# Optimization experiments

Measured on AMD Instinct MI355X. Metric: run time of the kernel, lower is better.

## Reference

```python
import jax, jax.numpy as jnp
import numpy as np

B, NWORD, HID = 4, 24, 512


def setup_inputs() -> dict:
    key = jax.random.key(0)
    ks = jax.random.split(key, 7)
    H = HID
    scale_in = 1.0 / np.sqrt(H)
    return {
        "seqt": jax.random.normal(ks[0], (B, NWORD, 2 * H), dtype=jnp.float32),
        # ins_input_linearity: Linear(H -> 5H) with bias
        "Wi": jax.random.normal(ks[1], (5 * H, H), dtype=jnp.float32) * scale_in,
        "bi": jnp.zeros((5 * H,), dtype=jnp.float32),
        # ins_state_linearity: Linear(H -> 5H) with bias (bias init: forget slots = 1)
        "Ws": jax.random.normal(ks[2], (5 * H, H), dtype=jnp.float32) * scale_in,
        "bs": jnp.zeros((5 * H,), dtype=jnp.float32).at[H:2 * H].set(1.0),
        # ins_bilinearity: BilinearSimilarity(2H, 2H) -> scalar x^T W y
        "Wbil": jax.random.normal(ks[3], (2 * H, 2 * H), dtype=jnp.float32) * (1.0 / (2.0 * H)),
    }


def reference(seqt, Wi, bi, Ws, bs, Wbil):
    """Inside pass (do_inside) of DioLstm in training mode (soft_sum over splits).

    Chart cell (left, L) covers words [left, left+L]. Returns root v = concat(h, c).
    """
    Bn, n, twoH = seqt.shape
    H = twoH // 2
    # ins_bias buffer: ones on the two forget-gate slots [H:3H]
    ins_bias = jnp.zeros((5 * H,), dtype=seqt.dtype).at[H:3 * H].set(1.0)

    def single(seq):  # seq: [n, 2H]
        chartH = jnp.zeros((n, n, H), seq.dtype).at[:, 0].set(seq[:, :H])
        chartC = jnp.zeros((n, n, H), seq.dtype).at[:, 0].set(seq[:, H:])
        chartS = jnp.zeros((n, n), seq.dtype)  # leaf scores are 0
        for L in range(1, n):  # span length - 1 (static unroll over diagonals)
            P = n - L  # number of spans on this diagonal
            lefts = jnp.arange(P)[:, None]          # [P,1]
            ksplit = jnp.arange(L)[None, :]          # [1,L]
            # left child: (left, k); right child: (left+k+1, L-1-k)
            lH = chartH[lefts, ksplit]; lC = chartC[lefts, ksplit]; lS = chartS[lefts, ksplit]
            ridx = lefts + ksplit + 1
            rlen = jnp.broadcast_to(L - 1 - ksplit, ridx.shape)
            rH = chartH[ridx, rlen]; rC = chartC[ridx, rlen]; rS = chartS[ridx, rlen]
            lv = jnp.concatenate([lH, lC], axis=-1)  # [P,L,2H]
            rv = jnp.concatenate([rH, rC], axis=-1)
            # bilinear compatibility + child scores
            compat = jnp.einsum('pki,ij,pkj->pk', lv, Wbil, rv) + lS + rS  # [P,L]
            # projected_input + projected_state (sum once; gate slices of the sum)
            proj = (lH @ Wi.T + bi + ins_bias) + (rH @ Ws.T + bs)  # [P,L,5H]
            ig, lf, rf, g, og = jnp.split(proj, 5, axis=-1)
            ig = jax.nn.sigmoid(ig); lf = jax.nn.sigmoid(lf); rf = jax.nn.sigmoid(rf)
            g = jnp.tanh(g); og = jax.nn.sigmoid(og)
            mem = lf * lC + rf * rC + ig * g
            h = og * jnp.tanh(mem)  # [P,L,H]
            # soft_sum: torch.tensor(s_set) detaches scores -> stop_gradient on weights
            sw = jax.lax.stop_gradient(compat)
            w = jax.nn.softmax(sw, axis=-1)  # [P,L]
            Hnew = jnp.einsum('pk,pkh->ph', w, h)
            Cnew = jnp.einsum('pk,pkh->ph', w, mem)
            Snew = jnp.sum(w * sw, axis=-1)
            pidx = jnp.arange(P)
            chartH = chartH.at[pidx, L].set(Hnew)
            chartC = chartC.at[pidx, L].set(Cnew)
            chartS = chartS.at[pidx, L].set(Snew)
        # root cell v = concat(h, c)
        return jnp.concatenate([chartH[0, n - 1], chartC[0, n - 1]], axis=0)

    return jax.vmap(single)(seqt)  # [B, 2H]
```

## Files before the change

kernel.cpp:

```cpp
#include <hip/hip_runtime.h>
#include <math.h>

#define NB 4
#define NW 24
#define H 512
#define H2 1024
#define H5 2560
#define NCELL 300
#define NEED_BYTES ((size_t)72<<20)

static float* g_buf = nullptr;
__attribute__((constructor)) static void dio_alloc_ws(){
  (void)hipMalloc((void**)&g_buf, NEED_BYTES);
}

typedef __attribute__((ext_vector_type(8))) short bf16x8;
typedef __attribute__((ext_vector_type(4))) float f32x4;
typedef unsigned short ushort_t;

__device__ __forceinline__ int coff(int l){ return l*NW - (l*(l-1))/2; }
__device__ __forceinline__ float sigm(float x){ return 1.f/(1.f+__expf(-x)); }
__device__ __forceinline__ float ftanh(float x){ return 1.f - 2.f/(__expf(2.f*x)+1.f); }

__device__ __forceinline__ ushort_t f2b(float x){
  unsigned int u = __float_as_uint(x);
  u += 0x7FFF + ((u>>16)&1);
  return (ushort_t)(u>>16);
}
__device__ __forceinline__ float b2f(ushort_t h){
  return __uint_as_float(((unsigned int)h)<<16);
}
__device__ __forceinline__ void split_store(ushort_t* __restrict__ ph,
                                            ushort_t* __restrict__ pl,
                                            size_t idx, float x){
  ushort_t h = f2b(x);
  ph[idx] = h;
  pl[idx] = f2b(x - b2f(h));
}

__device__ __forceinline__ float compat_dot(const float* __restrict__ cU,
                                            const float* __restrict__ cH,
                                            const float* __restrict__ cC,
                                            const float* __restrict__ cS,
                                            int lc, int rc, int lane){
  const float4* U4  = (const float4*)(cU + (size_t)lc*H2);
  const float4* Hr4 = (const float4*)(cH + (size_t)rc*H);
  const float4* Cr4 = (const float4*)(cC + (size_t)rc*H);
  float p = 0.f;
  #pragma unroll
  for (int it=0; it<2; it++){
    float4 u = U4[lane + 64*it], h = Hr4[lane + 64*it];
    p += u.x*h.x + u.y*h.y + u.z*h.z + u.w*h.w;
  }
  #pragma unroll
  for (int it=0; it<2; it++){
    float4 u = U4[128 + lane + 64*it], c = Cr4[lane + 64*it];
    p += u.x*c.x + u.y*c.y + u.z*c.z + u.w*c.w;
  }
  #pragma unroll
  for (int off=32; off>0; off>>=1) p += __shfl_down(p, off);
  return p + cS[lc] + cS[rc];
}

__global__ void k_init(const float* __restrict__ seqt,
                       const float* __restrict__ Wi, const float* __restrict__ Ws,
                       const float* __restrict__ Wbil,
                       ushort_t* __restrict__ WiBh, ushort_t* __restrict__ WiBl,
                       ushort_t* __restrict__ WsBh, ushort_t* __restrict__ WsBl,
                       ushort_t* __restrict__ WbilTh, ushort_t* __restrict__ WbilTl,
                       float* __restrict__ cH, float* __restrict__ cC, float* __restrict__ cS,
                       ushort_t* __restrict__ cHbh, ushort_t* __restrict__ cHbl,
                       ushort_t* __restrict__ cCbh, ushort_t* __restrict__ cCbl){
  const int blk = blockIdx.x, t = threadIdx.x;
  if (blk < 10240){
    int i = blk*256 + t;
    const int n = H5*H;
    if (i < n) split_store(WiBh, WiBl, i, Wi[i]);
    else       split_store(WsBh, WsBl, i-n, Ws[i-n]);
  } else if (blk < 11264){
    __shared__ float tile[32][33];
    int tb = blk - 10240;
    int tr = (tb>>5)*32, tc = (tb&31)*32;
    int tx = t & 31, ty = t >> 5;
    #pragma unroll
    for (int i=0;i<32;i+=8)
      tile[ty+i][tx] = Wbil[(size_t)(tr+ty+i)*H2 + tc+tx];
    __syncthreads();
    #pragma unroll
    for (int i=0;i<32;i+=8)
      split_store(WbilTh, WbilTl, (size_t)(tc+ty+i)*H2 + tr+tx, tile[tx][ty+i]);
  } else {
    int tid = (blk-11264)*256 + t;
    if (tid < NB*NW*H){
      int b = tid/(NW*H); int r = tid%(NW*H); int i = r/H; int d = r%H;
      size_t idx = (size_t)(b*NCELL + i)*H + d;
      float hv = seqt[(size_t)(b*NW+i)*H2 + d];
      float cv = seqt[(size_t)(b*NW+i)*H2 + H + d];
      cH[idx]=hv; cC[idx]=cv;
      split_store(cHbh,cHbl,idx,hv);
      split_store(cCbh,cCbl,idx,cv);
      if (d==0) cS[b*NCELL+i] = 0.f;
    }
  }
}

__device__ __forceinline__ void mfma3(f32x4& acc, bf16x8 ah, bf16x8 al,
                                      bf16x8 bh, bf16x8 bl){
  acc = __builtin_amdgcn_mfma_f32_16x16x32_bf16(ah, bh, acc, 0,0,0);
  acc = __builtin_amdgcn_mfma_f32_16x16x32_bf16(ah, bl, acc, 0,0,0);
  acc = __builtin_amdgcn_mfma_f32_16x16x32_bf16(al, bh, acc, 0,0,0);
}

__global__ void __launch_bounds__(512)
k_projN(const ushort_t* __restrict__ WiBh, const ushort_t* __restrict__ WiBl,
        const ushort_t* __restrict__ WsBh, const ushort_t* __restrict__ WsBl,
        const ushort_t* __restrict__ WbilTh, const ushort_t* __restrict__ WbilTl,
        const float* __restrict__ bi, const float* __restrict__ bs,
        const ushort_t* __restrict__ cHbh, const ushort_t* __restrict__ cHbl,
        const ushort_t* __restrict__ cCbh, const ushort_t* __restrict__ cCbl,
        float* __restrict__ cPI, float* __restrict__ cPS, float* __restrict__ cU,
        int d, int P)
{
  __shared__ f32x4 red[8][64];
  const int t = threadIdx.x, wave = t>>6, lane = t&63;
  const int jt = blockIdx.x;
  const int m0 = blockIdx.y*16;
  const int Mtot = NB*P;
  const int nm = min(16, Mtot-m0);

  int kind, j0;
  if (jt < 160){ kind=0; j0 = jt*16; }
  else if (jt < 320){ kind=1; j0 = (jt-160)*16; }
  else { kind=2; j0 = (jt-320)*16; }

  const int r = lane & 15;
  const int q = lane >> 4;

  int mg = m0 + (r < nm ? r : 0);
  const size_t arow = (size_t)((mg/P)*NCELL + coff(d) + mg%P)*H;

  f32x4 acc = {0.f,0.f,0.f,0.f};

  if (kind < 2){
    const ushort_t* bh_ = (kind==0 ? WiBh : WsBh) + (size_t)(j0+r)*H;
    const ushort_t* bl_ = (kind==0 ? WiBl : WsBl) + (size_t)(j0+r)*H;
    const int ks = wave*64 + q*8;
    bf16x8 fah[2], fal[2], fbh[2], fbl[2];
    #pragma unroll
    for (int s=0;s<2;s++){
      const int ko = ks + s*32;
      fah[s] = *(const bf16x8*)(cHbh + arow + ko);
      fal[s] = *(const bf16x8*)(cHbl + arow + ko);
      fbh[s] = *(const bf16x8*)(bh_ + ko);
      fbl[s] = *(const bf16x8*)(bl_ + ko);
    }
    #pragma unroll
    for (int s=0;s<2;s++) mfma3(acc, fah[s], fal[s], fbh[s], fbl[s]);
  } else {
    const ushort_t* bh_ = WbilTh + (size_t)(j0+r)*H2;
    const ushort_t* bl_ = WbilTl + (size_t)(j0+r)*H2;
    const ushort_t* ah_ = (wave<4 ? cHbh : cCbh) + arow;
    const ushort_t* al_ = (wave<4 ? cHbl : cCbl) + arow;
    const int kg0 = wave*128;
    const int ka0 = kg0 & 511;
    bf16x8 fah[4], fal[4], fbh[4], fbl[4];
    #pragma unroll
    for (int s=0;s<4;s++){
      const int so = s*32 + q*8;
      fah[s] = *(const bf16x8*)(ah_ + ka0 + so);
      fal[s] = *(const bf16x8*)(al_ + ka0 + so);
      fbh[s] = *(const bf16x8*)(bh_ + kg0 + so);
      fbl[s] = *(const bf16x8*)(bl_ + kg0 + so);
    }
    #pragma unroll
    for (int s=0;s<4;s++) mfma3(acc, fah[s], fal[s], fbh[s], fbl[s]);
  }

  red[wave][lane] = acc;
  __syncthreads();
  if (wave == 0){
    f32x4 s0=red[0][lane], s1=red[1][lane], s2=red[2][lane], s3=red[3][lane];
    f32x4 s4=red[4][lane], s5=red[5][lane], s6=red[6][lane], s7=red[7][lane];
    f32x4 tot = ((s0+s1)+(s2+s3)) + ((s4+s5)+(s6+s7));
    const int jo = j0 + r;
    float bias = 0.f;
    if (kind==0) bias = bi[jo] + ((jo>=H && jo<3*H)?1.f:0.f);
    else if (kind==1) bias = bs[jo];
    #pragma unroll
    for (int reg=0; reg<4; reg++){
      const int m = q*4 + reg;
      if (m < nm){
        const int mg2 = m0 + m;
        const size_t cell = (size_t)((mg2/P)*NCELL + coff(d) + mg2%P);
        const float v = tot[reg];
        if (kind==0)      cPI[cell*H5 + jo] = v + bias;
        else if (kind==1) cPS[cell*H5 + jo] = v + bias;
        else              cU [cell*H2 + jo] = v;
      }
    }
  }
}

__global__ void __launch_bounds__(256)
k_combine3(const float* __restrict__ cPI, const float* __restrict__ cPS,
           const float* __restrict__ cU,
           float* __restrict__ cH, float* __restrict__ cC, float* __restrict__ cS,
           ushort_t* __restrict__ cHbh, ushort_t* __restrict__ cHbl,
           ushort_t* __restrict__ cCbh, ushort_t* __restrict__ cCbl,
           const float* __restrict__ compatR, float* __restrict__ compatW,
           int L, int P){
  const int t = threadIdx.x;
  const int lane = t & 63;
  const int wave = t >> 6;
  const int nphase = NB*P*16;
  const int blk = blockIdx.x;

  if (blk >= nphase){
    const int P1 = P-1;
    const int nterm = L-1;
    int tid = (blk-nphase)*4 + wave;
    if (P1 > 0 && nterm > 0 && tid < NB*P1*nterm){
      int cell1 = tid / nterm;
      int k = 1 + tid % nterm;
      int b = cell1 / P1, left = cell1 % P1;
      int lc = b*NCELL + coff(k) + left;
      int rc = b*NCELL + coff(L-k) + left+k+1;
      float v = compat_dot(cU, cH, cC, cS, lc, rc, lane);
      if (lane==0) compatW[(b*NW + left)*NW + k] = v;
    }
    return;
  }

  const int cellid = blk >> 4;
  const int dg = blk & 15;
  const int b = cellid / P;
  const int left = cellid % P;
  __shared__ float compat_s[32];
  __shared__ float wts_s[32];
  __shared__ float S_s;
  __shared__ float partH[8][32];
  __shared__ float partC[8][32];

  if (wave == 0){
    int lc = b*NCELL + left;
    int rc = b*NCELL + coff(L-1) + left+1;
    float v = compat_dot(cU, cH, cC, cS, lc, rc, lane);
    if (lane==0) compat_s[0] = v;
  } else if (wave == 1 && L >= 2){
    int lc = b*NCELL + coff(L-1) + left;
    int rc = b*NCELL + left+L;
    float v = compat_dot(cU, cH, cC, cS, lc, rc, lane);
    if (lane==0) compat_s[L-1] = v;
  }
  if (t >= 1 && t <= L-2) compat_s[t] = compatR[(b*NW + left)*NW + t];
  __syncthreads();
  if (t==0){
    float mx = -1e30f;
    for (int k=0;k<L;k++) mx = fmaxf(mx, compat_s[k]);
    float den = 0.f;
    for (int k=0;k<L;k++){ float e = __expf(compat_s[k]-mx); wts_s[k]=e; den+=e; }
    float inv = 1.f/den, S = 0.f;
    for (int k=0;k<L;k++){ wts_s[k]*=inv; S += wts_s[k]*compat_s[k]; }
    S_s = S;
  }
  __syncthreads();
  const int dloc = t & 31;
  const int dim = dg*32 + dloc;
  const int kpar = t >> 5;
  float aH = 0.f, aC = 0.f;
  for (int k=kpar; k<L; k+=8){
    float wk = wts_s[k];
    int lc = b*NCELL + coff(k) + left;
    int rc = b*NCELL + coff(L-1-k) + left+k+1;
    const float* PI = cPI + (size_t)lc*H5;
    const float* PS = cPS + (size_t)rc*H5;
    float p0 = PI[dim]     + PS[dim];
    float p1 = PI[H+dim]   + PS[H+dim];
    float p2 = PI[2*H+dim] + PS[2*H+dim];
    float p3 = PI[3*H+dim] + PS[3*H+dim];
    float p4 = PI[4*H+dim] + PS[4*H+dim];
    float lcv = cC[(size_t)lc*H + dim];
    float rcv = cC[(size_t)rc*H + dim];
    float mem = sigm(p1)*lcv + sigm(p2)*rcv + sigm(p0)*ftanh(p3);
    float h = sigm(p4)*ftanh(mem);
    aH += wk*h; aC += wk*mem;
  }
  if (kpar > 0){ partH[kpar][dloc]=aH; partC[kpar][dloc]=aC; }
  __syncthreads();
  if (kpar == 0){
    #pragma unroll
    for (int q=1;q<8;q++){ aH += partH[q][dloc]; aC += partC[q][dloc]; }
    size_t nc = (size_t)(b*NCELL + coff(L) + left);
    cH[nc*H + dim] = aH;
    cC[nc*H + dim] = aC;
    split_store(cHbh,cHbl, nc*H + dim, aH);
    split_store(cCbh,cCbl, nc*H + dim, aC);
    if (t==0 && dg==0) cS[nc] = S_s;
  }
}

__global__ void k_out(const float* __restrict__ cH, const float* __restrict__ cC,
                      float* __restrict__ out){
  int tid = blockIdx.x*256+threadIdx.x;
  if (tid >= NB*H2) return;
  int b = tid>>10, d = tid&1023;
  int cell = b*NCELL + 299;
  out[tid] = (d<H) ? cH[(size_t)cell*H + d] : cC[(size_t)cell*H + (d-H)];
}

extern "C" void kernel_launch(void* const* d_in, const int* in_sizes, int n_in,
                              void* d_out, int out_size, void* d_ws, size_t ws_size,
                              hipStream_t stream){
  const float* seqt = (const float*)d_in[0];
  const float* Wi   = (const float*)d_in[1];
  const float* bi   = (const float*)d_in[2];
  const float* Ws   = (const float*)d_in[3];
  const float* bs   = (const float*)d_in[4];
  const float* Wbil = (const float*)d_in[5];
  float* out = (float*)d_out;

  float* p = (ws_size >= NEED_BYTES && g_buf == nullptr) ? (float*)d_ws : g_buf;
  float* cH  = p; p += (size_t)NB*NCELL*H;
  float* cC  = p; p += (size_t)NB*NCELL*H;
  float* cS  = p; p += (size_t)NB*NCELL;
  float* cPI = p; p += (size_t)NB*NCELL*H5;
  float* cPS = p; p += (size_t)NB*NCELL*H5;
  float* cU  = p; p += (size_t)NB*NCELL*H2;
  float* compatA = p; p += (size_t)NB*NW*NW;
  float* compatB = p; p += (size_t)NB*NW*NW;
  ushort_t* u = (ushort_t*)p;
  ushort_t* WiBh   = u; u += (size_t)H5*H;
  ushort_t* WiBl   = u; u += (size_t)H5*H;
  ushort_t* WsBh   = u; u += (size_t)H5*H;
  ushort_t* WsBl   = u; u += (size_t)H5*H;
  ushort_t* WbilTh = u; u += (size_t)H2*H2;
  ushort_t* WbilTl = u; u += (size_t)H2*H2;
  ushort_t* cHbh   = u; u += (size_t)NB*NCELL*H;
  ushort_t* cHbl   = u; u += (size_t)NB*NCELL*H;
  ushort_t* cCbh   = u; u += (size_t)NB*NCELL*H;
  ushort_t* cCbl   = u; u += (size_t)NB*NCELL*H;

  k_init<<<11456, 256, 0, stream>>>(seqt, Wi, Ws, Wbil,
      WiBh, WiBl, WsBh, WsBl, WbilTh, WbilTl,
      cH, cC, cS, cHbh, cHbl, cCbh, cCbl);

  k_projN<<<dim3(384, (NB*NW+15)/16), 512, 0, stream>>>(
      WiBh, WiBl, WsBh, WsBl, WbilTh, WbilTl, bi, bs,
      cHbh, cHbl, cCbh, cCbl, cPI, cPS, cU, 0, NW);
  for (int L=1; L<NW; L++){
    int P = NW - L;
    int P1 = P-1, nterm = L-1;
    int wblk = (P1>0 && nterm>0) ? (NB*P1*nterm + 3)/4 : 0;
    float* bufR = (L&1) ? compatA : compatB;
    float* bufW = (L&1) ? compatB : compatA;
    k_combine3<<<NB*P*16 + wblk, 256, 0, stream>>>(
        cPI, cPS, cU, cH, cC, cS, cHbh, cHbl, cCbh, cCbl,
        bufR, bufW, L, P);
    if (L < NW-1)
      k_projN<<<dim3(384, (NB*P+15)/16), 512, 0, stream>>>(
          WiBh, WiBl, WsBh, WsBl, WbilTh, WbilTl, bi, bs,
          cHbh, cHbl, cCbh, cCbl, cPI, cPS, cU, L, P);
  }
  k_out<<<16, 256, 0, stream>>>(cH, cC, out);
}
```

Baseline: 625.9 us.

## Fuse combine and projection per diagonal into persistent work-queue kernel with flags

Merges the per-diagonal combine kernel and the following projection kernel into one persistent kernel. Blocks pull items from an atomic counter: combine items first, then compat writes, then projection tiles. Each projection tile spin-waits on per-cell completion flags, so projection of finished cells overlaps with combines still running. This halves kernel launches and removes the full inter-kernel barrier, at the cost of atomics, spin-waiting, and 512-thread blocks now used for the combine work.

```diff
diff --git a/kernel.cpp b/kernel.cpp
--- a/kernel.cpp
+++ b/kernel.cpp
@@ -70,7 +70,8 @@
                        ushort_t* __restrict__ WbilTh, ushort_t* __restrict__ WbilTl,
                        float* __restrict__ cH, float* __restrict__ cC, float* __restrict__ cS,
                        ushort_t* __restrict__ cHbh, ushort_t* __restrict__ cHbl,
-                       ushort_t* __restrict__ cCbh, ushort_t* __restrict__ cCbl){
+                       ushort_t* __restrict__ cCbh, ushort_t* __restrict__ cCbl,
+                       int* __restrict__ flags, int* __restrict__ counters){
   const int blk = blockIdx.x, t = threadIdx.x;
   if (blk < 10240){
     int i = blk*256 + t;
@@ -89,7 +90,7 @@
     #pragma unroll
     for (int i=0;i<32;i+=8)
       split_store(WbilTh, WbilTl, (size_t)(tc+ty+i)*H2 + tr+tx, tile[tx][ty+i]);
-  } else {
+  } else if (blk < 11456){
     int tid = (blk-11264)*256 + t;
     if (tid < NB*NW*H){
       int b = tid/(NW*H); int r = tid%(NW*H); int i = r/H; int d = r%H;
@@ -101,6 +102,10 @@
       split_store(cCbh,cCbl,idx,cv);
       if (d==0) cS[b*NCELL+i] = 0.f;
     }
+  } else {
+    int idx = (blk-11456)*256 + t;
+    if (idx < NB*NCELL) flags[idx] = 0;
+    if (idx < NW) counters[idx] = 0;
   }
 }
 
@@ -111,20 +116,17 @@
   acc = __builtin_amdgcn_mfma_f32_16x16x32_bf16(al, bh, acc, 0,0,0);
 }
 
-__global__ void __launch_bounds__(512)
-k_projN(const ushort_t* __restrict__ WiBh, const ushort_t* __restrict__ WiBl,
+__device__ __forceinline__ void proj_item(
+        const ushort_t* __restrict__ WiBh, const ushort_t* __restrict__ WiBl,
         const ushort_t* __restrict__ WsBh, const ushort_t* __restrict__ WsBl,
         const ushort_t* __restrict__ WbilTh, const ushort_t* __restrict__ WbilTl,
         const float* __restrict__ bi, const float* __restrict__ bs,
         const ushort_t* __restrict__ cHbh, const ushort_t* __restrict__ cHbl,
         const ushort_t* __restrict__ cCbh, const ushort_t* __restrict__ cCbl,
         float* __restrict__ cPI, float* __restrict__ cPS, float* __restrict__ cU,
-        int d, int P)
+        f32x4 (*red)[64], int jt, int m0, int d, int P)
 {
-  __shared__ f32x4 red[8][64];
   const int t = threadIdx.x, wave = t>>6, lane = t&63;
-  const int jt = blockIdx.x;
-  const int m0 = blockIdx.y*16;
   const int Mtot = NB*P;
   const int nm = min(16, Mtot-m0);
 
@@ -201,102 +203,151 @@
   }
 }
 
-__global__ void __launch_bounds__(256)
-k_combine3(const float* __restrict__ cPI, const float* __restrict__ cPS,
-           const float* __restrict__ cU,
-           float* __restrict__ cH, float* __restrict__ cC, float* __restrict__ cS,
-           ushort_t* __restrict__ cHbh, ushort_t* __restrict__ cHbl,
-           ushort_t* __restrict__ cCbh, ushort_t* __restrict__ cCbl,
-           const float* __restrict__ compatR, float* __restrict__ compatW,
-           int L, int P){
+__global__ void __launch_bounds__(512)
+k_step(const ushort_t* __restrict__ WiBh, const ushort_t* __restrict__ WiBl,
+       const ushort_t* __restrict__ WsBh, const ushort_t* __restrict__ WsBl,
+       const ushort_t* __restrict__ WbilTh, const ushort_t* __restrict__ WbilTl,
+       const float* __restrict__ bi, const float* __restrict__ bs,
+       float* __restrict__ cH, float* __restrict__ cC, float* __restrict__ cS,
+       ushort_t* __restrict__ cHbh, ushort_t* __restrict__ cHbl,
+       ushort_t* __restrict__ cCbh, ushort_t* __restrict__ cCbl,
+       float* __restrict__ cPI, float* __restrict__ cPS, float* __restrict__ cU,
+       const float* __restrict__ compatR, float* __restrict__ compatW,
+       int* __restrict__ counters, int* __restrict__ flags,
+       int L, int P, int ncomb, int nwrit, int total)
+{
+  __shared__ int s_item;
+  __shared__ float compat_s[32];
+  __shared__ float wts_s[32];
+  __shared__ float S_s;
+  __shared__ float partH[16][32];
+  __shared__ float partC[16][32];
+  __shared__ f32x4 red[8][64];
   const int t = threadIdx.x;
   const int lane = t & 63;
   const int wave = t >> 6;
-  const int nphase = NB*P*16;
-  const int blk = blockIdx.x;
-
-  if (blk >= nphase){
-    const int P1 = P-1;
-    const int nterm = L-1;
-    int tid = (blk-nphase)*4 + wave;
-    if (P1 > 0 && nterm > 0 && tid < NB*P1*nterm){
-      int cell1 = tid / nterm;
-      int k = 1 + tid % nterm;
-      int b = cell1 / P1, left = cell1 % P1;
-      int lc = b*NCELL + coff(k) + left;
-      int rc = b*NCELL + coff(L-k) + left+k+1;
-      float v = compat_dot(cU, cH, cC, cS, lc, rc, lane);
-      if (lane==0) compatW[(b*NW + left)*NW + k] = v;
+
+  for(;;){
+    if (t==0) s_item = atomicAdd(&counters[L], 1);
+    __syncthreads();
+    const int item = s_item;
+    __syncthreads();
+    if (item >= total) return;
+
+    if (item < ncomb){
+      const int cellid = item >> 4;
+      const int dg = item & 15;
+      const int b = cellid / P;
+      const int left = cellid % P;
+      if (wave == 0){
+        int lc = b*NCELL + left;
+        int rc = b*NCELL + coff(L-1) + left+1;
+        float v = compat_dot(cU, cH, cC, cS, lc, rc, lane);
+        if (lane==0) compat_s[0] = v;
+      } else if (wave == 1 && L >= 2){
+        int lc = b*NCELL + coff(L-1) + left;
+        int rc = b*NCELL + left+L;
+        float v = compat_dot(cU, cH, cC, cS, lc, rc, lane);
+        if (lane==0) compat_s[L-1] = v;
+      }
+      if (t >= 1 && t <= L-2) compat_s[t] = compatR[(b*NW + left)*NW + t];
+      __syncthreads();
+      if (t==0){
+        float mx = -1e30f;
+        for (int k=0;k<L;k++) mx = fmaxf(mx, compat_s[k]);
+        float den = 0.f;
+        for (int k=0;k<L;k++){ float e = __expf(compat_s[k]-mx); wts_s[k]=e; den+=e; }
+        float inv = 1.f/den, S = 0.f;
+        for (int k=0;k<L;k++){ wts_s[k]*=inv; S += wts_s[k]*compat_s[k]; }
+        S_s = S;
+      }
+      __syncthreads();
+      const int dloc = t & 31;
+      const int dim = dg*32 + dloc;
+      const int kpar = t >> 5;
+      float aH = 0.f, aC = 0.f;
+      for (int k=kpar; k<L; k+=16){
+        float wk = wts_s[k];
+        int lc = b*NCELL + coff(k) + left;
+        int rc = b*NCELL + coff(L-1-k) + left+k+1;
+        const float* PI = cPI + (size_t)lc*H5;
+        const float* PS = cPS + (size_t)rc*H5;
+        float p0 = PI[dim]     + PS[dim];
+        float p1 = PI[H+dim]   + PS[H+dim];
+        float p2 = PI[2*H+dim] + PS[2*H+dim];
+        float p3 = PI[3*H+dim] + PS[3*H+dim];
+        float p4 = PI[4*H+dim] + PS[4*H+dim];
+        float lcv = cC[(size_t)lc*H + dim];
+        float rcv = cC[(size_t)rc*H + dim];
+        float mem = sigm(p1)*lcv + sigm(p2)*rcv + sigm(p0)*ftanh(p3);
+        float h = sigm(p4)*ftanh(mem);
+        aH += wk*h; aC += wk*mem;
+      }
+      if (kpar > 0){ partH[kpar][dloc]=aH; partC[kpar][dloc]=aC; }
+      __syncthreads();
+      const size_t nc = (size_t)(b*NCELL + coff(L) + left);
+      if (kpar == 0){
+        #pragma unroll
+        for (int q=1;q<16;q++){ aH += partH[q][dloc]; aC += partC[q][dloc]; }
+        cH[nc*H + dim] = aH;
+        cC[nc*H + dim] = aC;
+        split_store(cHbh,cHbl, nc*H + dim, aH);
+        split_store(cCbh,cCbl, nc*H + dim, aC);
+        if (t==0 && dg==0) cS[nc] = S_s;
+      }
+      __syncthreads();
+      if (t==0){
+        __threadfence();
+        atomicAdd(&flags[nc], 1);
+      }
+      __syncthreads();
+    } else if (item < ncomb + nwrit){
+      const int P1 = P-1;
+      const int nterm = L-1;
+      int tid = (item-ncomb)*8 + wave;
+      if (tid < NB*P1*nterm){
+        int cell1 = tid / nterm;
+        int k = 1 + tid % nterm;
+        int b = cell1 / P1, left = cell1 % P1;
+        int lc = b*NCELL + coff(k) + left;
+        int rc = b*NCELL + coff(L-k) + left+k+1;
+        float v = compat_dot(cU, cH, cC, cS, lc, rc, lane);
+        if (lane==0) compatW[(b*NW + left)*NW + k] = v;
+      }
+      __syncthreads();
+    } else {
+      const int pidx = item - ncomb - nwrit;
+      const int jt = pidx % 384;
+      const int m0 = (pidx / 384) * 16;
+      const int Mtot = NB*P;
+      const int nm = min(16, Mtot-m0);
+      if (t < 16){
+        int mg = m0 + (t < nm ? t : 0);
+        int cell = (mg/P)*NCELL + coff(L) + mg%P;
+        while (atomicAdd(&flags[cell], 0) < 16) {}
+      }
+      asm volatile("" ::: "memory");
+      __syncthreads();
+      proj_item(WiBh,WiBl,WsBh,WsBl,WbilTh,WbilTl,bi,bs,
+                cHbh,cHbl,cCbh,cCbl,cPI,cPS,cU, red, jt, m0, L, P);
+      __syncthreads();
     }
-    return;
-  }
-
-  const int cellid = blk >> 4;
-  const int dg = blk & 15;
-  const int b = cellid / P;
-  const int left = cellid % P;
-  __shared__ float compat_s[32];
-  __shared__ float wts_s[32];
-  __shared__ float S_s;
-  __shared__ float partH[8][32];
-  __shared__ float partC[8][32];
-
-  if (wave == 0){
-    int lc = b*NCELL + left;
-    int rc = b*NCELL + coff(L-1) + left+1;
-    float v = compat_dot(cU, cH, cC, cS, lc, rc, lane);
-    if (lane==0) compat_s[0] = v;
-  } else if (wave == 1 && L >= 2){
-    int lc = b*NCELL + coff(L-1) + left;
-    int rc = b*NCELL + left+L;
-    float v = compat_dot(cU, cH, cC, cS, lc, rc, lane);
-    if (lane==0) compat_s[L-1] = v;
-  }
-  if (t >= 1 && t <= L-2) compat_s[t] = compatR[(b*NW + left)*NW + t];
-  __syncthreads();
-  if (t==0){
-    float mx = -1e30f;
-    for (int k=0;k<L;k++) mx = fmaxf(mx, compat_s[k]);
-    float den = 0.f;
-    for (int k=0;k<L;k++){ float e = __expf(compat_s[k]-mx); wts_s[k]=e; den+=e; }
-    float inv = 1.f/den, S = 0.f;
-    for (int k=0;k<L;k++){ wts_s[k]*=inv; S += wts_s[k]*compat_s[k]; }
-    S_s = S;
-  }
-  __syncthreads();
-  const int dloc = t & 31;
-  const int dim = dg*32 + dloc;
-  const int kpar = t >> 5;
-  float aH = 0.f, aC = 0.f;
-  for (int k=kpar; k<L; k+=8){
-    float wk = wts_s[k];
-    int lc = b*NCELL + coff(k) + left;
-    int rc = b*NCELL + coff(L-1-k) + left+k+1;
-    const float* PI = cPI + (size_t)lc*H5;
-    const float* PS = cPS + (size_t)rc*H5;
-    float p0 = PI[dim]     + PS[dim];
-    float p1 = PI[H+dim]   + PS[H+dim];
-    float p2 = PI[2*H+dim] + PS[2*H+dim];
-    float p3 = PI[3*H+dim] + PS[3*H+dim];
-    float p4 = PI[4*H+dim] + PS[4*H+dim];
-    float lcv = cC[(size_t)lc*H + dim];
-    float rcv = cC[(size_t)rc*H + dim];
-    float mem = sigm(p1)*lcv + sigm(p2)*rcv + sigm(p0)*ftanh(p3);
-    float h = sigm(p4)*ftanh(mem);
-    aH += wk*h; aC += wk*mem;
-  }
-  if (kpar > 0){ partH[kpar][dloc]=aH; partC[kpar][dloc]=aC; }
-  __syncthreads();
-  if (kpar == 0){
-    #pragma unroll
-    for (int q=1;q<8;q++){ aH += partH[q][dloc]; aC += partC[q][dloc]; }
-    size_t nc = (size_t)(b*NCELL + coff(L) + left);
-    cH[nc*H + dim] = aH;
-    cC[nc*H + dim] = aC;
-    split_store(cHbh,cHbl, nc*H + dim, aH);
-    split_store(cCbh,cCbl, nc*H + dim, aC);
-    if (t==0 && dg==0) cS[nc] = S_s;
-  }
+  }
+}
+
+__global__ void __launch_bounds__(512)
+k_proj0(const ushort_t* __restrict__ WiBh, const ushort_t* __restrict__ WiBl,
+        const ushort_t* __restrict__ WsBh, const ushort_t* __restrict__ WsBl,
+        const ushort_t* __restrict__ WbilTh, const ushort_t* __restrict__ WbilTl,
+        const float* __restrict__ bi, const float* __restrict__ bs,
+        const ushort_t* __restrict__ cHbh, const ushort_t* __restrict__ cHbl,
+        const ushort_t* __restrict__ cCbh, const ushort_t* __restrict__ cCbl,
+        float* __restrict__ cPI, float* __restrict__ cPS, float* __restrict__ cU)
+{
+  __shared__ f32x4 red[8][64];
+  proj_item(WiBh,WiBl,WsBh,WsBl,WbilTh,WbilTl,bi,bs,
+            cHbh,cHbl,cCbh,cCbl,cPI,cPS,cU, red,
+            blockIdx.x, blockIdx.y*16, 0, NW);
 }
 
 __global__ void k_out(const float* __restrict__ cH, const float* __restrict__ cC,
@@ -328,6 +379,8 @@
   float* cU  = p; p += (size_t)NB*NCELL*H2;
   float* compatA = p; p += (size_t)NB*NW*NW;
   float* compatB = p; p += (size_t)NB*NW*NW;
+  int* flags    = (int*)p; p += NB*NCELL;
+  int* counters = (int*)p; p += NW;
   ushort_t* u = (ushort_t*)p;
   ushort_t* WiBh   = u; u += (size_t)H5*H;
   ushort_t* WiBl   = u; u += (size_t)H5*H;
@@ -340,26 +393,28 @@
   ushort_t* cCbh   = u; u += (size_t)NB*NCELL*H;
   ushort_t* cCbl   = u; u += (size_t)NB*NCELL*H;
 
-  k_init<<<11456, 256, 0, stream>>>(seqt, Wi, Ws, Wbil,
+  k_init<<<11461, 256, 0, stream>>>(seqt, Wi, Ws, Wbil,
       WiBh, WiBl, WsBh, WsBl, WbilTh, WbilTl,
-      cH, cC, cS, cHbh, cHbl, cCbh, cCbl);
-
-  k_projN<<<dim3(384, (NB*NW+15)/16), 512, 0, stream>>>(
+      cH, cC, cS, cHbh, cHbl, cCbh, cCbl, flags, counters);
+
+  k_proj0<<<dim3(384, (NB*NW+15)/16), 512, 0, stream>>>(
       WiBh, WiBl, WsBh, WsBl, WbilTh, WbilTl, bi, bs,
-      cHbh, cHbl, cCbh, cCbl, cPI, cPS, cU, 0, NW);
+      cHbh, cHbl, cCbh, cCbl, cPI, cPS, cU);
+
   for (int L=1; L<NW; L++){
     int P = NW - L;
+    int ncomb = NB*P*16;
     int P1 = P-1, nterm = L-1;
-    int wblk = (P1>0 && nterm>0) ? (NB*P1*nterm + 3)/4 : 0;
+    int nwrit = (P1>0 && nterm>0) ? (NB*P1*nterm + 7)/8 : 0;
+    int nproj = (L < NW-1) ? 384*((NB*P+15)/16) : 0;
+    int total = ncomb + nwrit + nproj;
+    int grid = total < 1024 ? total : 1024;
     float* bufR = (L&1) ? compatA : compatB;
     float* bufW = (L&1) ? compatB : compatA;
-    k_combine3<<<NB*P*16 + wblk, 256, 0, stream>>>(
-        cPI, cPS, cU, cH, cC, cS, cHbh, cHbl, cCbh, cCbl,
-        bufR, bufW, L, P);
-    if (L < NW-1)
-      k_projN<<<dim3(384, (NB*P+15)/16), 512, 0, stream>>>(
-          WiBh, WiBl, WsBh, WsBl, WbilTh, WbilTl, bi, bs,
-          cHbh, cHbl, cCbh, cCbl, cPI, cPS, cU, L, P);
+    k_step<<<grid, 512, 0, stream>>>(
+        WiBh, WiBl, WsBh, WsBl, WbilTh, WbilTl, bi, bs,
+        cH, cC, cS, cHbh, cHbl, cCbh, cCbl, cPI, cPS, cU,
+        bufR, bufW, counters, flags, L, P, ncomb, nwrit, total);
   }
   k_out<<<16, 256, 0, stream>>>(cH, cC, out);
 }
```

New measurement: 1.457 ms. 133% more time.

## Widen combine kernel to 512 threads with per-split threads and block-wide boundary dots

Applied to the files above, without the earlier changes.

Doubles the combine block size to 512 threads and halves the dims per block (16 instead of 32), so each split k gets its own thread group rather than looping with stride 8. The two boundary bilinear dot products are now computed by all 512 threads with float4 loads and wave reductions, rather than by a single wave each. The intent is shorter per-block latency on this latency-bound diagonal loop. The cost is twice as many blocks, which doubles the redundant boundary-dot and softmax work done per cell, plus a 32-way shared-memory reduction.

```diff
diff --git a/kernel.cpp b/kernel.cpp
--- a/kernel.cpp
+++ b/kernel.cpp
@@ -201,8 +201,8 @@
   }
 }
 
-__global__ void __launch_bounds__(256)
-k_combine3(const float* __restrict__ cPI, const float* __restrict__ cPS,
+__global__ void __launch_bounds__(512)
+k_combine4(const float* __restrict__ cPI, const float* __restrict__ cPS,
            const float* __restrict__ cU,
            float* __restrict__ cH, float* __restrict__ cC, float* __restrict__ cS,
            ushort_t* __restrict__ cHbh, ushort_t* __restrict__ cHbl,
@@ -212,13 +212,13 @@
   const int t = threadIdx.x;
   const int lane = t & 63;
   const int wave = t >> 6;
-  const int nphase = NB*P*16;
+  const int nphase = NB*P*32;
   const int blk = blockIdx.x;
 
   if (blk >= nphase){
     const int P1 = P-1;
     const int nterm = L-1;
-    int tid = (blk-nphase)*4 + wave;
+    int tid = (blk-nphase)*8 + wave;
     if (P1 > 0 && nterm > 0 && tid < NB*P1*nterm){
       int cell1 = tid / nterm;
       int k = 1 + tid % nterm;
@@ -231,30 +231,46 @@
     return;
   }
 
-  const int cellid = blk >> 4;
-  const int dg = blk & 15;
+  const int cellid = blk >> 5;
+  const int dg = blk & 31;
   const int b = cellid / P;
   const int left = cellid % P;
   __shared__ float compat_s[32];
   __shared__ float wts_s[32];
   __shared__ float S_s;
-  __shared__ float partH[8][32];
-  __shared__ float partC[8][32];
-
-  if (wave == 0){
-    int lc = b*NCELL + left;
-    int rc = b*NCELL + coff(L-1) + left+1;
-    float v = compat_dot(cU, cH, cC, cS, lc, rc, lane);
-    if (lane==0) compat_s[0] = v;
-  } else if (wave == 1 && L >= 2){
-    int lc = b*NCELL + coff(L-1) + left;
-    int rc = b*NCELL + left+L;
-    float v = compat_dot(cU, cH, cC, cS, lc, rc, lane);
-    if (lane==0) compat_s[L-1] = v;
+  __shared__ float bnd[8];
+  __shared__ float partH[32][16];
+  __shared__ float partC[32][16];
+
+  {
+    const int half = t >> 8;
+    const int pr = t & 255;
+    int lc, rc;
+    if (half==0){ lc = b*NCELL + left;                rc = b*NCELL + coff(L-1) + left+1; }
+    else        { lc = b*NCELL + coff(L-1) + left;    rc = b*NCELL + left+L; }
+    float pp = 0.f;
+    if (half==0 || L>=2){
+      float4 u = ((const float4*)(cU + (size_t)lc*H2))[pr];
+      float4 x = (pr < 128)
+               ? ((const float4*)(cH + (size_t)rc*H))[pr]
+               : ((const float4*)(cC + (size_t)rc*H))[pr-128];
+      pp = u.x*x.x + u.y*x.y + u.z*x.z + u.w*x.w;
+    }
+    #pragma unroll
+    for (int off=32; off>0; off>>=1) pp += __shfl_down(pp, off);
+    if (lane==0) bnd[wave] = pp;
   }
   if (t >= 1 && t <= L-2) compat_s[t] = compatR[(b*NW + left)*NW + t];
   __syncthreads();
   if (t==0){
+    {
+      int lc = b*NCELL + left, rc = b*NCELL + coff(L-1) + left+1;
+      compat_s[0] = ((bnd[0]+bnd[1])+(bnd[2]+bnd[3])) + cS[lc] + cS[rc];
+    }
+    if (L >= 2){
+      int lc = b*NCELL + coff(L-1) + left, rc = b*NCELL + left+L;
+      compat_s[L-1] = ((bnd[4]+bnd[5])+(bnd[6]+bnd[7])) + cS[lc] + cS[rc];
+    }
     float mx = -1e30f;
     for (int k=0;k<L;k++) mx = fmaxf(mx, compat_s[k]);
     float den = 0.f;
@@ -264,11 +280,12 @@
     S_s = S;
   }
   __syncthreads();
-  const int dloc = t & 31;
-  const int dim = dg*32 + dloc;
-  const int kpar = t >> 5;
+  const int dloc = t & 15;
+  const int dim = dg*16 + dloc;
+  const int kpar = t >> 4;
   float aH = 0.f, aC = 0.f;
-  for (int k=kpar; k<L; k+=8){
+  if (kpar < L){
+    const int k = kpar;
     float wk = wts_s[k];
     int lc = b*NCELL + coff(k) + left;
     int rc = b*NCELL + coff(L-1-k) + left+k+1;
@@ -283,13 +300,13 @@
     float rcv = cC[(size_t)rc*H + dim];
     float mem = sigm(p1)*lcv + sigm(p2)*rcv + sigm(p0)*ftanh(p3);
     float h = sigm(p4)*ftanh(mem);
-    aH += wk*h; aC += wk*mem;
+    aH = wk*h; aC = wk*mem;
   }
   if (kpar > 0){ partH[kpar][dloc]=aH; partC[kpar][dloc]=aC; }
   __syncthreads();
   if (kpar == 0){
     #pragma unroll
-    for (int q=1;q<8;q++){ aH += partH[q][dloc]; aC += partC[q][dloc]; }
+    for (int q=1;q<32;q++){ aH += partH[q][dloc]; aC += partC[q][dloc]; }
     size_t nc = (size_t)(b*NCELL + coff(L) + left);
     cH[nc*H + dim] = aH;
     cC[nc*H + dim] = aC;
@@ -350,10 +367,10 @@
   for (int L=1; L<NW; L++){
     int P = NW - L;
     int P1 = P-1, nterm = L-1;
-    int wblk = (P1>0 && nterm>0) ? (NB*P1*nterm + 3)/4 : 0;
+    int wblk = (P1>0 && nterm>0) ? (NB*P1*nterm + 7)/8 : 0;
     float* bufR = (L&1) ? compatA : compatB;
     float* bufW = (L&1) ? compatB : compatA;
-    k_combine3<<<NB*P*16 + wblk, 256, 0, stream>>>(
+    k_combine4<<<NB*P*32 + wblk, 512, 0, stream>>>(
         cPI, cPS, cU, cH, cC, cS, cHbh, cHbl, cCbh, cCbl,
         bufR, bufW, L, P);
     if (L < NW-1)
```

Result: slower. 683.7 us (+9.2%).
